# Performance work log

Measured on AMD Instinct MI355X. Metric: run time of the kernel, lower is better.

The kernel has to match this reference:

```python
import jax, jax.numpy as jnp
import numpy as np
import math

N_HEADS = 8

def setup_inputs() -> dict:
    key = jax.random.key(0)
    qkv = jax.random.normal(key, (4, 1536, 2048), dtype=jnp.float32)
    return {"qkv": qkv}

def reference(qkv):
    bs, width, length = qkv.shape
    ch = width // (3 * N_HEADS)
    # reshape to [bs*n_heads, 3*ch, length] then split into q, k, v
    qkv_h = qkv.reshape(bs * N_HEADS, 3 * ch, length)
    q = qkv_h[:, :ch]
    k = qkv_h[:, ch:2 * ch]
    v = qkv_h[:, 2 * ch:]
    scale = 1.0 / math.sqrt(math.sqrt(ch))
    # scores: [B*H, T, S]
    weight = jnp.einsum('bct,bcs->bts', q * scale, k * scale)
    weight = jax.nn.softmax(weight.astype(jnp.float32), axis=-1).astype(weight.dtype)
    a = jnp.einsum('bts,bcs->bct', weight, v)  # [B*H, ch, T]
    return a.reshape(bs, N_HEADS * ch, length)
```

## Files before the change

### kernel.cpp

```cpp
#include <hip/hip_runtime.h>
#include <hip/hip_bf16.h>

typedef __attribute__((ext_vector_type(8))) short bf16x8;
typedef __attribute__((ext_vector_type(8))) unsigned short u16x8;
typedef __attribute__((ext_vector_type(4))) float f32x4;
typedef __attribute__((ext_vector_type(16))) float f32x16;

#define SEQ 2048
#define NBH 32
#define QSCALE 0.1803368801111204f

#if __has_builtin(__builtin_amdgcn_exp2f)
#define EXP2(x) __builtin_amdgcn_exp2f(x)
#else
#define EXP2(x) exp2f(x)
#endif

__device__ __forceinline__ unsigned short bfc(float f) {
  union { __hip_bfloat16 h; unsigned short u; } v;
  v.h = __float2bfloat16(f);
  return v.u;
}

__device__ __forceinline__ void gl_lds16(const void* g, void* l) {
  __builtin_amdgcn_global_load_lds((__attribute__((address_space(1))) void*)g,
                                   (__attribute__((address_space(3))) void*)l, 16, 0, 0);
}

__global__ __launch_bounds__(256)
void prep_kernel(const float* __restrict__ qkv, unsigned short* __restrict__ ws) {
  const int tid = threadIdx.x;
  const int b = blockIdx.x;
  if (b < 4096) {
    int gid = b * 256 + tid;
    int sec = gid >> 19;
    int r = gid & 524287;
    int bh = r >> 14;
    int rr = r & 16383;
    int cc = rr >> 11;
    int t = rr & 2047;
    const float* src = qkv + ((size_t)(bh >> 3) * 1536 + (bh & 7) * 192 + sec * 64 + cc * 8) * SEQ + t;
    const float scale = sec ? 1.0f : QSCALE;
    u16x8 o;
    #pragma unroll
    for (int e = 0; e < 8; ++e) o[e] = bfc(src[(size_t)e * SEQ] * scale);
    unsigned short* dst = ws + ((size_t)sec * NBH * SEQ + (size_t)bh * SEQ + t) * 64;
    *(u16x8*)(dst + ((cc ^ (t & 7)) * 8)) = o;
  } else {
    int cid = (b - 4096) * 256 + tid;
    int bh = cid >> 14;
    int rr = cid & 16383;
    int c = rr >> 8;
    int cc = rr & 255;
    int grp = cc >> 3, sub = cc & 7;
    const float* src = qkv + ((size_t)(bh >> 3) * 1536 + (bh & 7) * 192 + 128 + c) * SEQ + cc * 8;
    float4 a = *(const float4*)(src);
    float4 bv = *(const float4*)(src + 4);
    u16x8 o;
    o[0] = bfc(a.x); o[1] = bfc(a.y); o[2] = bfc(a.z); o[3] = bfc(a.w);
    o[4] = bfc(bv.x); o[5] = bfc(bv.y); o[6] = bfc(bv.z); o[7] = bfc(bv.w);
    unsigned short* dst = ws + (size_t)2 * NBH * SEQ * 64 +
                          ((size_t)bh * 64 + c) * SEQ + grp * 64 + ((sub ^ (c & 7)) * 8);
    *(u16x8*)dst = o;
  }
}

__global__ __launch_bounds__(512, 1)
void attn_main(const unsigned short* __restrict__ ws, float* __restrict__ out) {
  const int bid = blockIdx.x;
  const int bh = (bid & 7) + 8 * ((bid >> 3) >> 3);
  const int tile = (bid >> 3) & 7;
  const int t0 = tile * 256;

  const unsigned short* Qws = ws + ((size_t)bh * SEQ + t0) * 64;
  const unsigned short* Kws = ws + (size_t)NBH * SEQ * 64 + (size_t)bh * SEQ * 64;
  const unsigned short* Vws = ws + (size_t)2 * NBH * SEQ * 64 + (size_t)bh * 64 * SEQ;
  float* __restrict__ outb = out + (size_t)bh * 64 * SEQ;

  __shared__ __align__(16) char smem[98304];
  unsigned short* QP = (unsigned short*)smem;
  unsigned short* KtB = (unsigned short*)(smem + 32768);
  unsigned short* VtB = (unsigned short*)(smem + 65536);

  const int tid = threadIdx.x;
  const int w = tid >> 6;
  const int ts = w & 3;
  const int sh = w >> 2;
  const int l = tid & 63;
  const int lw = l & 31;
  const int h = l >> 5;
  const int sw = lw & 7;

  #pragma unroll
  for (int i = 0; i < 4; ++i)
    gl_lds16(Qws + (size_t)(tid + i * 512) * 8, &QP[(tid + i * 512) * 8]);
  gl_lds16(Kws + (size_t)tid * 8, &KtB[tid * 8]);
  gl_lds16(Kws + (size_t)(tid + 512) * 8, &KtB[(tid + 512) * 8]);
  {
    int q = tid;       int c = q >> 4, g2 = (q >> 3) & 1, j = q & 7;
    gl_lds16(Vws + (size_t)c * SEQ + g2 * 64 + j * 8, &VtB[q * 8]);
    q = tid + 512;     c = q >> 4;     g2 = (q >> 3) & 1; j = q & 7;
    gl_lds16(Vws + (size_t)c * SEQ + g2 * 64 + j * 8, &VtB[q * 8]);
  }
  __syncthreads();

  bf16x8 qB[2][4];
  #pragma unroll
  for (int tsub = 0; tsub < 2; ++tsub) {
    const int rloc = ts * 64 + tsub * 32 + lw;
    #pragma unroll
    for (int kc = 0; kc < 4; ++kc)
      qB[tsub][kc] = *(const bf16x8*)&QP[rloc * 64 + (((2 * kc + h) ^ sw) * 8)];
  }

  f32x16 zero16;
  #pragma unroll
  for (int i = 0; i < 16; ++i) zero16[i] = 0.f;
  bf16x8 onesB;
  #pragma unroll
  for (int i = 0; i < 8; ++i) onesB[i] = (short)0x3F80;

  f32x16 accO[2][2];
  f32x16 psum[2];
  accO[0][0] = zero16; accO[0][1] = zero16;
  accO[1][0] = zero16; accO[1][1] = zero16;
  psum[0] = zero16; psum[1] = zero16;

  int cur = 0;
  #pragma unroll 1
  for (int it = 0; it < SEQ / 128; ++it) {
    const int s1 = (it + 1) & 15;
    {
      const unsigned short* kn = Kws + (size_t)s1 * 8192;
      unsigned short* kd = KtB + (cur ^ 1) * 8192;
      gl_lds16(kn + (size_t)tid * 8, &kd[tid * 8]);
      gl_lds16(kn + (size_t)(tid + 512) * 8, &kd[(tid + 512) * 8]);
      unsigned short* vd = VtB + (cur ^ 1) * 8192;
      int q = tid;     int c = q >> 4, g2 = (q >> 3) & 1, j = q & 7;
      gl_lds16(Vws + (size_t)c * SEQ + (2 * s1 + g2) * 64 + j * 8, &vd[q * 8]);
      q = tid + 512;   c = q >> 4;     g2 = (q >> 3) & 1; j = q & 7;
      gl_lds16(Vws + (size_t)c * SEQ + (2 * s1 + g2) * 64 + j * 8, &vd[q * 8]);
    }

    const unsigned short* kb = KtB + cur * 8192;
    const unsigned short* vb = VtB + cur * 8192;

    f32x16 accS[2][2];
    #pragma unroll
    for (int ms = 0; ms < 2; ++ms) {
      #pragma unroll
      for (int kc = 0; kc < 4; ++kc) {
        bf16x8 ka = *(const bf16x8*)&kb[(sh * 64 + 32 * ms + lw) * 64 + (((2 * kc + h) ^ sw) * 8)];
        #pragma unroll
        for (int tsub = 0; tsub < 2; ++tsub)
          accS[ms][tsub] = __builtin_amdgcn_mfma_f32_32x32x16_bf16(
              ka, qB[tsub][kc], kc ? accS[ms][tsub] : zero16, 0, 0, 0);
      }
    }

    #pragma unroll
    for (int ms = 0; ms < 2; ++ms)
      #pragma unroll
      for (int tsub = 0; tsub < 2; ++tsub)
        #pragma unroll
        for (int r = 0; r < 16; ++r) accS[ms][tsub][r] = EXP2(accS[ms][tsub][r]);

    bf16x8 pA[2][4];
    #pragma unroll
    for (int tsub = 0; tsub < 2; ++tsub) {
      #pragma unroll
      for (int ms = 0; ms < 2; ++ms) {
        unsigned int pk[8];
        #pragma unroll
        for (int wd = 0; wd < 8; ++wd)
          asm("v_cvt_pk_bf16_f32 %0, %1, %2"
              : "=v"(pk[wd]) : "v"(accS[ms][tsub][2 * wd]), "v"(accS[ms][tsub][2 * wd + 1]));
        #pragma unroll
        for (int a = 0; a < 2; ++a) {
          unsigned int x0 = pk[4 * a + 0], y0 = pk[4 * a + 2];
          unsigned int x1 = pk[4 * a + 1], y1 = pk[4 * a + 3];
          asm("v_permlane32_swap_b32 %0, %1" : "+v"(x0), "+v"(y0));
          asm("v_permlane32_swap_b32 %0, %1" : "+v"(x1), "+v"(y1));
          union { unsigned int u[4]; bf16x8 v; } uu;
          uu.u[0] = x0; uu.u[1] = x1; uu.u[2] = y0; uu.u[3] = y1;
          pA[tsub][2 * ms + a] = uu.v;
        }
      }
    }

    #pragma unroll
    for (int tsub = 0; tsub < 2; ++tsub)
      #pragma unroll
      for (int ks = 0; ks < 4; ++ks)
        psum[tsub] = __builtin_amdgcn_mfma_f32_32x32x16_bf16(pA[tsub][ks], onesB, psum[tsub], 0, 0, 0);

    #pragma unroll
    for (int ch = 0; ch < 2; ++ch) {
      #pragma unroll
      for (int ks = 0; ks < 4; ++ks) {
        bf16x8 vB = *(const bf16x8*)&vb[(32 * ch + lw) * 128 + sh * 64 + (((2 * ks + h) ^ sw) * 8)];
        #pragma unroll
        for (int tsub = 0; tsub < 2; ++tsub)
          accO[tsub][ch] = __builtin_amdgcn_mfma_f32_32x32x16_bf16(pA[tsub][ks], vB, accO[tsub][ch], 0, 0, 0);
      }
    }

    __syncthreads();
    cur ^= 1;
  }

  float* cO = (float*)smem;
  float* cP = (float*)(smem + 65536);
  if (sh == 1) {
    #pragma unroll
    for (int tsub = 0; tsub < 2; ++tsub) {
      #pragma unroll
      for (int ch = 0; ch < 2; ++ch)
        #pragma unroll
        for (int r = 0; r < 16; ++r)
          cO[ts * 4096 + (tsub * 2 + ch) * 1024 + r * 64 + l] = accO[tsub][ch][r];
      #pragma unroll
      for (int r = 0; r < 16; ++r)
        cP[ts * 2048 + tsub * 1024 + r * 64 + l] = psum[tsub][r];
    }
  }
  __syncthreads();
  if (sh == 0) {
    #pragma unroll
    for (int tsub = 0; tsub < 2; ++tsub) {
      #pragma unroll
      for (int r = 0; r < 16; ++r)
        psum[tsub][r] += cP[ts * 2048 + tsub * 1024 + r * 64 + l];
      float linv[16];
      #pragma unroll
      for (int r = 0; r < 16; ++r) linv[r] = 1.0f / psum[tsub][r];
      #pragma unroll
      for (int ch = 0; ch < 2; ++ch) {
        #pragma unroll
        for (int r = 0; r < 16; ++r) {
          float v = accO[tsub][ch][r] + cO[ts * 4096 + (tsub * 2 + ch) * 1024 + r * 64 + l];
          const int tg = t0 + ts * 64 + tsub * 32 + (r & 3) + 8 * (r >> 2) + 4 * h;
          outb[(size_t)(32 * ch + lw) * SEQ + tg] = v * linv[r];
        }
      }
    }
  }
}

#define PAD 72
#define BTF 128
__device__ __forceinline__ unsigned short f2bf(float f) {
  union { float f; unsigned u; } v; v.f = f;
  return (unsigned short)((v.u + 0x7fffu + ((v.u >> 16) & 1u)) >> 16);
}

__global__ __launch_bounds__(512, 4)
void qkv_attn_fallback(const float* __restrict__ qkv, float* __restrict__ out) {
  const int bid = blockIdx.x;
  const int xcd = bid & 7;
  const int slot = bid >> 3;
  const int bh = xcd + 8 * (slot >> 4);
  const int tile = slot & 15;
  const int t0 = tile * BTF;

  const float* __restrict__ base = qkv + (size_t)((bh >> 3) * 1536 + (bh & 7) * 192) * SEQ;
  const float* __restrict__ qg = base;
  const float* __restrict__ kg = base + 64 * SEQ;
  const float* __restrict__ vg = base + 128 * SEQ;
  float* __restrict__ outb = out + (size_t)bh * 64 * SEQ;

  __shared__ __align__(16) unsigned short Qt[BTF * PAD];
  __shared__ __align__(16) unsigned short Kt[64 * PAD];
  __shared__ __align__(16) unsigned short Vt[64 * PAD];
  __shared__ __align__(16) unsigned short Pl[BTF * PAD];

  const int tid = threadIdx.x;
  const int w = tid >> 6;
  const int l = tid & 63;
  const int lr = l & 15;
  const int g = l >> 4;

  {
    const int cb = tid >> 5, tb = tid & 31;
    const int c0 = cb * 4, tt0 = tb * 4;
    const float* p = qg + c0 * SEQ + t0 + tt0;
    float4 r0 = *(const float4*)(p);
    float4 r1 = *(const float4*)(p + SEQ);
    float4 r2 = *(const float4*)(p + 2 * SEQ);
    float4 r3 = *(const float4*)(p + 3 * SEQ);
    const float s = 0.125f;
    ushort4 w0 = { f2bf(r0.x*s), f2bf(r1.x*s), f2bf(r2.x*s), f2bf(r3.x*s) };
    ushort4 w1 = { f2bf(r0.y*s), f2bf(r1.y*s), f2bf(r2.y*s), f2bf(r3.y*s) };
    ushort4 w2 = { f2bf(r0.z*s), f2bf(r1.z*s), f2bf(r2.z*s), f2bf(r3.z*s) };
    ushort4 w3 = { f2bf(r0.w*s), f2bf(r1.w*s), f2bf(r2.w*s), f2bf(r3.w*s) };
    *(ushort4*)&Qt[(tt0 + 0) * PAD + c0] = w0;
    *(ushort4*)&Qt[(tt0 + 1) * PAD + c0] = w1;
    *(ushort4*)&Qt[(tt0 + 2) * PAD + c0] = w2;
    *(ushort4*)&Qt[(tt0 + 3) * PAD + c0] = w3;
  }
  __syncthreads();

  bf16x8 qB0 = *(const bf16x8*)&Qt[(w * 16 + lr) * PAD + g * 8];
  bf16x8 qB1 = *(const bf16x8*)&Qt[(w * 16 + lr) * PAD + g * 8 + 32];

  f32x4 pv[4];
  #pragma unroll
  for (int i = 0; i < 4; ++i) pv[i] = (f32x4){0.f, 0.f, 0.f, 0.f};
  float mrun = -1e30f;
  float lsum = 0.f;

  for (int s0 = 0; s0 < SEQ; s0 += 64) {
    __syncthreads();
    {
      const int cb = tid >> 4, sb = tid & 15;
      const int c0 = cb * 2, sl = sb * 4;
      const float* p0 = kg + c0 * SEQ + s0 + sl;
      float4 a0 = *(const float4*)(p0);
      float4 a1 = *(const float4*)(p0 + SEQ);
      ushort2 y0 = { f2bf(a0.x), f2bf(a1.x) };
      ushort2 y1 = { f2bf(a0.y), f2bf(a1.y) };
      ushort2 y2 = { f2bf(a0.z), f2bf(a1.z) };
      ushort2 y3 = { f2bf(a0.w), f2bf(a1.w) };
      *(ushort2*)&Kt[(sl + 0) * PAD + c0] = y0;
      *(ushort2*)&Kt[(sl + 1) * PAD + c0] = y1;
      *(ushort2*)&Kt[(sl + 2) * PAD + c0] = y2;
      *(ushort2*)&Kt[(sl + 3) * PAD + c0] = y3;
    }
    {
      const int c = tid >> 3;
      const int sq = (tid & 7) * 8;
      const float* p0 = vg + c * SEQ + s0 + sq;
      float4 b0 = *(const float4*)(p0);
      float4 b1 = *(const float4*)(p0 + 4);
      ushort4 z0 = { f2bf(b0.x), f2bf(b0.y), f2bf(b0.z), f2bf(b0.w) };
      ushort4 z1 = { f2bf(b1.x), f2bf(b1.y), f2bf(b1.z), f2bf(b1.w) };
      *(ushort4*)&Vt[c * PAD + sq] = z0;
      *(ushort4*)&Vt[c * PAD + sq + 4] = z1;
    }
    __syncthreads();

    f32x4 acc[4];
    #pragma unroll
    for (int i = 0; i < 4; ++i) acc[i] = (f32x4){0.f, 0.f, 0.f, 0.f};
    #pragma unroll
    for (int ch = 0; ch < 2; ++ch) {
      bf16x8 qb = ch ? qB1 : qB0;
      #pragma unroll
      for (int sub = 0; sub < 4; ++sub) {
        bf16x8 ka = *(const bf16x8*)&Kt[(sub * 16 + lr) * PAD + g * 8 + 32 * ch];
        acc[sub] = __builtin_amdgcn_mfma_f32_16x16x32_bf16(ka, qb, acc[sub], 0, 0, 0);
      }
    }

    float pmax = -1e30f;
    #pragma unroll
    for (int sub = 0; sub < 4; ++sub)
      #pragma unroll
      for (int r = 0; r < 4; ++r) pmax = fmaxf(pmax, acc[sub][r]);
    pmax = fmaxf(pmax, __shfl_xor(pmax, 16));
    pmax = fmaxf(pmax, __shfl_xor(pmax, 32));
    const float mnew = fmaxf(mrun, pmax);
    const float alpha = __expf(mrun - mnew);
    float rsum = 0.f;
    #pragma unroll
    for (int sub = 0; sub < 4; ++sub) {
      #pragma unroll
      for (int r = 0; r < 4; ++r) {
        float p = __expf(acc[sub][r] - mnew);
        acc[sub][r] = p;
        rsum += p;
      }
    }
    rsum += __shfl_xor(rsum, 16);
    rsum += __shfl_xor(rsum, 32);
    lsum = lsum * alpha + rsum;
    mrun = mnew;

    #pragma unroll
    for (int sub = 0; sub < 4; ++sub) {
      ushort4 pw = { f2bf(acc[sub][0]), f2bf(acc[sub][1]), f2bf(acc[sub][2]), f2bf(acc[sub][3]) };
      *(ushort4*)&Pl[(w * 16 + lr) * PAD + sub * 16 + g * 4] = pw;
    }

    {
      const int sbase = (l & 48) + g * 4;
      #pragma unroll
      for (int r = 0; r < 4; ++r) {
        float ar = __shfl(alpha, sbase + r, 64);
        #pragma unroll
        for (int cs = 0; cs < 4; ++cs) pv[cs][r] *= ar;
      }
    }

    bf16x8 pA0 = *(const bf16x8*)&Pl[(w * 16 + lr) * PAD + g * 8];
    bf16x8 pA1 = *(const bf16x8*)&Pl[(w * 16 + lr) * PAD + g * 8 + 32];
    #pragma unroll
    for (int cs = 0; cs < 4; ++cs) {
      bf16x8 v0 = *(const bf16x8*)&Vt[(cs * 16 + lr) * PAD + g * 8];
      bf16x8 v1 = *(const bf16x8*)&Vt[(cs * 16 + lr) * PAD + g * 8 + 32];
      pv[cs] = __builtin_amdgcn_mfma_f32_16x16x32_bf16(pA0, v0, pv[cs], 0, 0, 0);
      pv[cs] = __builtin_amdgcn_mfma_f32_16x16x32_bf16(pA1, v1, pv[cs], 0, 0, 0);
    }
  }

  {
    const int sbase = (l & 48) + g * 4;
    float linv[4];
    #pragma unroll
    for (int r = 0; r < 4; ++r) linv[r] = 1.0f / __shfl(lsum, sbase + r, 64);
    #pragma unroll
    for (int cs = 0; cs < 4; ++cs) {
      #pragma unroll
      for (int r = 0; r < 4; ++r) {
        outb[(cs * 16 + lr) * SEQ + t0 + w * 16 + g * 4 + r] = pv[cs][r] * linv[r];
      }
    }
  }
}

extern "C" void kernel_launch(void* const* d_in, const int* in_sizes, int n_in,
                              void* d_out, int out_size, void* d_ws, size_t ws_size,
                              hipStream_t stream) {
  const float* qkv = (const float*)d_in[0];
  float* out = (float*)d_out;
  const size_t need = (size_t)3 * NBH * SEQ * 64 * sizeof(unsigned short);
  if (ws_size >= need) {
    unsigned short* ws = (unsigned short*)d_ws;
    prep_kernel<<<dim3(6144), dim3(256), 0, stream>>>(qkv, ws);
    attn_main<<<dim3(256), dim3(512), 0, stream>>>(ws, out);
  } else {
    qkv_attn_fallback<<<dim3(512), dim3(512), 0, stream>>>(qkv, out);
  }
}
```

Measured before the change: 58.37 us.

## Halve query tile per block and split keys four ways across waves

Each block now covers 128 query rows instead of 256, and the grid doubles to 512 blocks, so all CUs on the device get work. Waves are arranged as 2 query groups by 4 key splits. The O and row-sum partials are reduced across the four splits through LDS in two passes over the channel halves. Q fragments are loaded straight from global memory into registers rather than staged through LDS, which cuts LDS to 64KB. In exchange, K and V are streamed twice as many times in total, and the final reduction needs more barriers.

```diff
diff --git a/kernel.cpp b/kernel.cpp
--- a/kernel.cpp
+++ b/kernel.cpp
@@ -68,32 +68,37 @@
 __global__ __launch_bounds__(512, 1)
 void attn_main(const unsigned short* __restrict__ ws, float* __restrict__ out) {
   const int bid = blockIdx.x;
-  const int bh = (bid & 7) + 8 * ((bid >> 3) >> 3);
-  const int tile = (bid >> 3) & 7;
-  const int t0 = tile * 256;
+  const int bh = (bid & 7) + 8 * ((bid >> 3) >> 4);
+  const int tile = (bid >> 3) & 15;
+  const int t0 = tile * 128;
 
   const unsigned short* Qws = ws + ((size_t)bh * SEQ + t0) * 64;
   const unsigned short* Kws = ws + (size_t)NBH * SEQ * 64 + (size_t)bh * SEQ * 64;
   const unsigned short* Vws = ws + (size_t)2 * NBH * SEQ * 64 + (size_t)bh * 64 * SEQ;
   float* __restrict__ outb = out + (size_t)bh * 64 * SEQ;
 
-  __shared__ __align__(16) char smem[98304];
-  unsigned short* QP = (unsigned short*)smem;
-  unsigned short* KtB = (unsigned short*)(smem + 32768);
-  unsigned short* VtB = (unsigned short*)(smem + 65536);
+  __shared__ __align__(16) char smem[65536];
+  unsigned short* KtB = (unsigned short*)smem;
+  unsigned short* VtB = (unsigned short*)(smem + 32768);
 
   const int tid = threadIdx.x;
   const int w = tid >> 6;
-  const int ts = w & 3;
-  const int sh = w >> 2;
+  const int ts = w & 1;
+  const int sh = w >> 1;
   const int l = tid & 63;
   const int lw = l & 31;
   const int h = l >> 5;
   const int sw = lw & 7;
 
+  bf16x8 qB[2][4];
   #pragma unroll
-  for (int i = 0; i < 4; ++i)
-    gl_lds16(Qws + (size_t)(tid + i * 512) * 8, &QP[(tid + i * 512) * 8]);
+  for (int tsub = 0; tsub < 2; ++tsub) {
+    const int rloc = ts * 64 + tsub * 32 + lw;
+    #pragma unroll
+    for (int kc = 0; kc < 4; ++kc)
+      qB[tsub][kc] = *(const bf16x8*)&Qws[rloc * 64 + (((2 * kc + h) ^ sw) * 8)];
+  }
+
   gl_lds16(Kws + (size_t)tid * 8, &KtB[tid * 8]);
   gl_lds16(Kws + (size_t)(tid + 512) * 8, &KtB[(tid + 512) * 8]);
   {
@@ -104,15 +109,6 @@
   }
   __syncthreads();
 
-  bf16x8 qB[2][4];
-  #pragma unroll
-  for (int tsub = 0; tsub < 2; ++tsub) {
-    const int rloc = ts * 64 + tsub * 32 + lw;
-    #pragma unroll
-    for (int kc = 0; kc < 4; ++kc)
-      qB[tsub][kc] = *(const bf16x8*)&QP[rloc * 64 + (((2 * kc + h) ^ sw) * 8)];
-  }
-
   f32x16 zero16;
   #pragma unroll
   for (int i = 0; i < 16; ++i) zero16[i] = 0.f;
@@ -129,8 +125,8 @@
   int cur = 0;
   #pragma unroll 1
   for (int it = 0; it < SEQ / 128; ++it) {
-    const int s1 = (it + 1) & 15;
     {
+      const int s1 = (it + 1) & 15;
       const unsigned short* kn = Kws + (size_t)s1 * 8192;
       unsigned short* kd = KtB + (cur ^ 1) * 8192;
       gl_lds16(kn + (size_t)tid * 8, &kd[tid * 8]);
@@ -145,60 +141,53 @@
     const unsigned short* kb = KtB + cur * 8192;
     const unsigned short* vb = VtB + cur * 8192;
 
-    f32x16 accS[2][2];
-    #pragma unroll
-    for (int ms = 0; ms < 2; ++ms) {
-      #pragma unroll
-      for (int kc = 0; kc < 4; ++kc) {
-        bf16x8 ka = *(const bf16x8*)&kb[(sh * 64 + 32 * ms + lw) * 64 + (((2 * kc + h) ^ sw) * 8)];
-        #pragma unroll
-        for (int tsub = 0; tsub < 2; ++tsub)
-          accS[ms][tsub] = __builtin_amdgcn_mfma_f32_32x32x16_bf16(
-              ka, qB[tsub][kc], kc ? accS[ms][tsub] : zero16, 0, 0, 0);
-      }
-    }
-
-    #pragma unroll
-    for (int ms = 0; ms < 2; ++ms)
+    f32x16 accS[2];
+    #pragma unroll
+    for (int kc = 0; kc < 4; ++kc) {
+      bf16x8 ka = *(const bf16x8*)&kb[(sh * 32 + lw) * 64 + (((2 * kc + h) ^ sw) * 8)];
       #pragma unroll
       for (int tsub = 0; tsub < 2; ++tsub)
-        #pragma unroll
-        for (int r = 0; r < 16; ++r) accS[ms][tsub][r] = EXP2(accS[ms][tsub][r]);
-
-    bf16x8 pA[2][4];
+        accS[tsub] = __builtin_amdgcn_mfma_f32_32x32x16_bf16(
+            ka, qB[tsub][kc], kc ? accS[tsub] : zero16, 0, 0, 0);
+    }
+
+    #pragma unroll
+    for (int tsub = 0; tsub < 2; ++tsub)
+      #pragma unroll
+      for (int r = 0; r < 16; ++r) accS[tsub][r] = EXP2(accS[tsub][r]);
+
+    bf16x8 pA[2][2];
     #pragma unroll
     for (int tsub = 0; tsub < 2; ++tsub) {
-      #pragma unroll
-      for (int ms = 0; ms < 2; ++ms) {
-        unsigned int pk[8];
-        #pragma unroll
-        for (int wd = 0; wd < 8; ++wd)
-          asm("v_cvt_pk_bf16_f32 %0, %1, %2"
-              : "=v"(pk[wd]) : "v"(accS[ms][tsub][2 * wd]), "v"(accS[ms][tsub][2 * wd + 1]));
-        #pragma unroll
-        for (int a = 0; a < 2; ++a) {
-          unsigned int x0 = pk[4 * a + 0], y0 = pk[4 * a + 2];
-          unsigned int x1 = pk[4 * a + 1], y1 = pk[4 * a + 3];
-          asm("v_permlane32_swap_b32 %0, %1" : "+v"(x0), "+v"(y0));
-          asm("v_permlane32_swap_b32 %0, %1" : "+v"(x1), "+v"(y1));
-          union { unsigned int u[4]; bf16x8 v; } uu;
-          uu.u[0] = x0; uu.u[1] = x1; uu.u[2] = y0; uu.u[3] = y1;
-          pA[tsub][2 * ms + a] = uu.v;
-        }
+      unsigned int pk[8];
+      #pragma unroll
+      for (int wd = 0; wd < 8; ++wd)
+        asm("v_cvt_pk_bf16_f32 %0, %1, %2"
+            : "=v"(pk[wd]) : "v"(accS[tsub][2 * wd]), "v"(accS[tsub][2 * wd + 1]));
+      #pragma unroll
+      for (int a = 0; a < 2; ++a) {
+        unsigned int x0 = pk[4 * a + 0], y0 = pk[4 * a + 2];
+        unsigned int x1 = pk[4 * a + 1], y1 = pk[4 * a + 3];
+        asm("v_permlane32_swap_b32 %0, %1" : "+v"(x0), "+v"(y0));
+        asm("v_permlane32_swap_b32 %0, %1" : "+v"(x1), "+v"(y1));
+        union { unsigned int u[4]; bf16x8 v; } uu;
+        uu.u[0] = x0; uu.u[1] = x1; uu.u[2] = y0; uu.u[3] = y1;
+        pA[tsub][a] = uu.v;
       }
     }
 
     #pragma unroll
     for (int tsub = 0; tsub < 2; ++tsub)
       #pragma unroll
-      for (int ks = 0; ks < 4; ++ks)
+      for (int ks = 0; ks < 2; ++ks)
         psum[tsub] = __builtin_amdgcn_mfma_f32_32x32x16_bf16(pA[tsub][ks], onesB, psum[tsub], 0, 0, 0);
 
     #pragma unroll
     for (int ch = 0; ch < 2; ++ch) {
       #pragma unroll
-      for (int ks = 0; ks < 4; ++ks) {
-        bf16x8 vB = *(const bf16x8*)&vb[(32 * ch + lw) * 128 + sh * 64 + (((2 * ks + h) ^ sw) * 8)];
+      for (int ks = 0; ks < 2; ++ks) {
+        bf16x8 vB = *(const bf16x8*)&vb[(32 * ch + lw) * 128 + (sh >> 1) * 64 +
+                                        (((((sh & 1) * 4) + 2 * ks + h) ^ sw) * 8)];
         #pragma unroll
         for (int tsub = 0; tsub < 2; ++tsub)
           accO[tsub][ch] = __builtin_amdgcn_mfma_f32_32x32x16_bf16(pA[tsub][ks], vB, accO[tsub][ch], 0, 0, 0);
@@ -209,38 +198,55 @@
     cur ^= 1;
   }
 
-  float* cO = (float*)smem;
-  float* cP = (float*)(smem + 65536);
-  if (sh == 1) {
-    #pragma unroll
-    for (int tsub = 0; tsub < 2; ++tsub) {
-      #pragma unroll
-      for (int ch = 0; ch < 2; ++ch)
+  float* red = (float*)smem;
+  #pragma unroll
+  for (int ch = 0; ch < 2; ++ch) {
+    __syncthreads();
+    if (sh != 0) {
+      #pragma unroll
+      for (int tsub = 0; tsub < 2; ++tsub)
         #pragma unroll
         for (int r = 0; r < 16; ++r)
-          cO[ts * 4096 + (tsub * 2 + ch) * 1024 + r * 64 + l] = accO[tsub][ch][r];
+          red[((((sh - 1) * 2 + ts) * 2 + tsub) * 16 + r) * 64 + l] = accO[tsub][ch][r];
+    }
+    __syncthreads();
+    if (sh == 0) {
+      #pragma unroll
+      for (int tsub = 0; tsub < 2; ++tsub)
+        #pragma unroll
+        for (int r = 0; r < 16; ++r)
+          #pragma unroll
+          for (int p = 0; p < 3; ++p)
+            accO[tsub][ch][r] += red[(((p * 2 + ts) * 2 + tsub) * 16 + r) * 64 + l];
+    }
+  }
+  __syncthreads();
+  if (sh != 0) {
+    #pragma unroll
+    for (int tsub = 0; tsub < 2; ++tsub)
       #pragma unroll
       for (int r = 0; r < 16; ++r)
-        cP[ts * 2048 + tsub * 1024 + r * 64 + l] = psum[tsub][r];
-    }
+        red[((((sh - 1) * 2 + ts) * 2 + tsub) * 16 + r) * 64 + l] = psum[tsub][r];
   }
   __syncthreads();
   if (sh == 0) {
     #pragma unroll
     for (int tsub = 0; tsub < 2; ++tsub) {
-      #pragma unroll
-      for (int r = 0; r < 16; ++r)
-        psum[tsub][r] += cP[ts * 2048 + tsub * 1024 + r * 64 + l];
       float linv[16];
       #pragma unroll
-      for (int r = 0; r < 16; ++r) linv[r] = 1.0f / psum[tsub][r];
+      for (int r = 0; r < 16; ++r) {
+        float pt = psum[tsub][r];
+        #pragma unroll
+        for (int p = 0; p < 3; ++p)
+          pt += red[(((p * 2 + ts) * 2 + tsub) * 16 + r) * 64 + l];
+        linv[r] = 1.0f / pt;
+      }
       #pragma unroll
       for (int ch = 0; ch < 2; ++ch) {
         #pragma unroll
         for (int r = 0; r < 16; ++r) {
-          float v = accO[tsub][ch][r] + cO[ts * 4096 + (tsub * 2 + ch) * 1024 + r * 64 + l];
           const int tg = t0 + ts * 64 + tsub * 32 + (r & 3) + 8 * (r >> 2) + 4 * h;
-          outb[(size_t)(32 * ch + lw) * SEQ + tg] = v * linv[r];
+          outb[(size_t)(32 * ch + lw) * SEQ + tg] = accO[tsub][ch][r] * linv[r];
         }
       }
     }
@@ -427,7 +433,7 @@
   if (ws_size >= need) {
     unsigned short* ws = (unsigned short*)d_ws;
     prep_kernel<<<dim3(6144), dim3(256), 0, stream>>>(qkv, ws);
-    attn_main<<<dim3(256), dim3(512), 0, stream>>>(ws, out);
+    attn_main<<<dim3(512), dim3(512), 0, stream>>>(ws, out);
   } else {
     qkv_attn_fallback<<<dim3(512), dim3(512), 0, stream>>>(qkv, out);
   }
```

Measured after the change: 65.49 us. 1.12x slower.
